# Kernel tuning notes

Measured on AMD Instinct MI355X. Metric: run time of the kernel, lower is better.

The kernel has to match this reference:

```python
import jax, jax.numpy as jnp
import numpy as np

V, H_BASE, D, L, K = 32000, 4096, 512, 2, 4
B = 64

def setup_inputs() -> dict:
    key = jax.random.key(0)
    ks = jax.random.split(key, 12)
    s = 0.02
    return {
        "hidden_state": jax.random.normal(ks[0], (B, H_BASE), jnp.float32),
        "in_proj_w": jax.random.normal(ks[1], (D, H_BASE), jnp.float32) * s,
        "in_proj_b": jnp.zeros((D,), jnp.float32),
        "w_ih0": jax.random.normal(ks[2], (3 * D, D), jnp.float32) * s,
        "w_hh0": jax.random.normal(ks[3], (3 * D, D), jnp.float32) * s,
        "b_ih0": jax.random.normal(ks[4], (3 * D,), jnp.float32) * s,
        "b_hh0": jax.random.normal(ks[5], (3 * D,), jnp.float32) * s,
        "w_ih1": jax.random.normal(ks[6], (3 * D, D), jnp.float32) * s,
        "w_hh1": jax.random.normal(ks[7], (3 * D, D), jnp.float32) * s,
        "b_ih1": jax.random.normal(ks[8], (3 * D,), jnp.float32) * s,
        "b_hh1": jax.random.normal(ks[9], (3 * D,), jnp.float32) * s,
        "embed": jax.random.normal(ks[10], (V, D), jnp.float32) * s,
        "out_w": jax.random.normal(ks[11], (V, D), jnp.float32) * s,
    }

def _gru_cell(x, h, w_ih, w_hh, b_ih, b_hh):
    # PyTorch GRU gate order: r, z, n
    gi = x @ w_ih.T + b_ih  # [B, 3D]
    gh = h @ w_hh.T + b_hh
    ir, iz, inn = jnp.split(gi, 3, axis=-1)
    hr, hz, hn = jnp.split(gh, 3, axis=-1)
    r = jax.nn.sigmoid(ir + hr)
    z = jax.nn.sigmoid(iz + hz)
    n = jnp.tanh(inn + r * hn)
    return (1.0 - z) * n + z * h

def reference(hidden_state, in_proj_w, in_proj_b, w_ih0, w_hh0, b_ih0, b_hh0,
              w_ih1, w_hh1, b_ih1, b_hh1, embed, out_w):
    b = hidden_state.shape[0]
    h0 = hidden_state @ in_proj_w.T + in_proj_b  # [B, D]
    h_l0 = h0
    h_l1 = h0
    x = jnp.zeros((b, in_proj_w.shape[0]), hidden_state.dtype)
    all_logits = []
    for _ in range(K):
        h_l0 = _gru_cell(x, h_l0, w_ih0, w_hh0, b_ih0, b_hh0)
        h_l1 = _gru_cell(h_l0, h_l1, w_ih1, w_hh1, b_ih1, b_hh1)
        logits = h_l1 @ out_w.T  # [B, V]
        all_logits.append(logits)
        x = embed[jnp.argmax(logits, axis=-1)]  # greedy next-token embed
    return jnp.stack(all_logits, axis=1)  # [B, K, V]
```

## Files before the change

### kernel.cpp

```cpp
#include <hip/hip_runtime.h>
#include <math.h>


typedef __attribute__((ext_vector_type(8))) short short8;
typedef __attribute__((ext_vector_type(4))) float f32x4;

__device__ __forceinline__ unsigned short f2bf_rne(float x) {
    unsigned u = __float_as_uint(x);
    unsigned r = (u + 0x7fffu + ((u >> 16) & 1u)) >> 16;
    return (unsigned short)r;
}
__device__ __forceinline__ void split2(float x, unsigned short& hi, unsigned short& lo) {
    unsigned u = __float_as_uint(x);
    hi = (unsigned short)(u >> 16);
    float r = x - __uint_as_float(u & 0xffff0000u);
    lo = f2bf_rne(r);
}

__device__ __forceinline__ void store_plane(unsigned short* hiP, unsigned short* loP,
                                            int m, int d, float v) {
    int s = d >> 6, cl = (d >> 3) & 7, e = d & 7;
    int off = m * 512 + s * 64 + ((cl ^ (m & 7)) * 8) + e;
    unsigned short hi, lo; split2(v, hi, lo);
    hiP[off] = hi; loP[off] = lo;
}

__device__ __forceinline__ void gload16(const void* g, void* lds) {
    __builtin_amdgcn_global_load_lds(
        (const __attribute__((address_space(1))) unsigned int*)g,
        (__attribute__((address_space(3))) unsigned int*)lds, 16, 0, 0);
}

__device__ __forceinline__ void split_w_body(
    const float* __restrict__ W, unsigned short* __restrict__ H,
    unsigned short* __restrict__ L, size_t g, int kclog)
{
    int n  = (int)(g >> kclog);
    int c8 = (int)g & ((1 << kclog) - 1);
    const float* src = W + g * 8;
    float4 v0 = *(const float4*)src;
    float4 v1 = *(const float4*)(src + 4);
    unsigned short h[8], l[8];
    split2(v0.x,h[0],l[0]); split2(v0.y,h[1],l[1]); split2(v0.z,h[2],l[2]); split2(v0.w,h[3],l[3]);
    split2(v1.x,h[4],l[4]); split2(v1.y,h[5],l[5]); split2(v1.z,h[6],l[6]); split2(v1.w,h[7],l[7]);
    uint4 ph = make_uint4((unsigned)h[0]|((unsigned)h[1]<<16), (unsigned)h[2]|((unsigned)h[3]<<16),
                          (unsigned)h[4]|((unsigned)h[5]<<16), (unsigned)h[6]|((unsigned)h[7]<<16));
    uint4 pl = make_uint4((unsigned)l[0]|((unsigned)l[1]<<16), (unsigned)l[2]|((unsigned)l[3]<<16),
                          (unsigned)l[4]|((unsigned)l[5]<<16), (unsigned)l[6]|((unsigned)l[7]<<16));
    int nt = n >> 7, row = n & 127;
    int ksi = c8 >> 3;
    int slot = (c8 & 7) ^ (row & 7);
    int tpr = 1 << (kclog - 3);
    size_t off = ((size_t)(nt * tpr + ksi) * 128 + row) * 64 + slot * 8;
    *(uint4*)(H + off) = ph;
    *(uint4*)(L + off) = pl;
}

__global__ __launch_bounds__(256) void k_split_W(
    const float* __restrict__ W, unsigned short* __restrict__ H,
    unsigned short* __restrict__ L, int kclog)
{
    size_t g = (size_t)blockIdx.x * 256 + threadIdx.x;
    split_w_body(W, H, L, g, kclog);
}

__global__ __launch_bounds__(256) void k_split_gw(
    const float* __restrict__ w0, const float* __restrict__ w1,
    const float* __restrict__ w2, const float* __restrict__ w3,
    unsigned short* __restrict__ H, unsigned short* __restrict__ L)
{
    int mat = blockIdx.y;
    const float* W = mat == 0 ? w0 : mat == 1 ? w1 : mat == 2 ? w2 : w3;
    size_t g = (size_t)blockIdx.x * 256 + threadIdx.x;
    split_w_body(W, H + (size_t)mat * 786432, L + (size_t)mat * 786432, g, 6);
}

template<bool ARGMAX>
__device__ __forceinline__ void mfma_gemm(
    const char* __restrict__ AH, const char* __restrict__ AL, int AstrideB, int akk0,
    const unsigned short* __restrict__ BH, const unsigned short* __restrict__ BL,
    size_t btileU,
    int nk,
    float* __restrict__ C, int ldc, int n0,
    unsigned short (*AsH)[4096], unsigned short (*AsL)[4096],
    unsigned short (*BsH)[8192], unsigned short (*BsL)[8192],
    float* __restrict__ pval, int* __restrict__ pidx, int bx)
{
    const int tid  = threadIdx.x;
    const int wv   = tid >> 6;
    const int lane = tid & 63;
    const int lr   = lane & 15;
    const int lh   = lane >> 4;
    const int m    = tid >> 3;
    const int cp   = tid & 7;

    f32x4 acc[4];
#pragma unroll
    for (int i = 0; i < 4; ++i) acc[i] = (f32x4){0.f, 0.f, 0.f, 0.f};

    auto stage = [&](int t, int p) {
        const int ka = (akk0 + t * 64) * 2;
        gload16(AH + m * AstrideB + ka + cp * 16, (char*)AsH[p] + wv * 1024);
        gload16(AL + m * AstrideB + ka + cp * 16, (char*)AsL[p] + wv * 1024);
        const char* bH = (const char*)BH + (btileU + (size_t)t * 8192) * 2;
        const char* bL = (const char*)BL + (btileU + (size_t)t * 8192) * 2;
        gload16(bH + wv * 2048 +        lane * 16, (char*)BsH[p] + wv * 2048);
        gload16(bH + wv * 2048 + 1024 + lane * 16, (char*)BsH[p] + wv * 2048 + 1024);
        gload16(bL + wv * 2048 +        lane * 16, (char*)BsL[p] + wv * 2048);
        gload16(bL + wv * 2048 + 1024 + lane * 16, (char*)BsL[p] + wv * 2048 + 1024);
    };

    stage(0, 0);
    __syncthreads();

    for (int t = 0; t < nk; ++t) {
        const int p = t & 1;
        if (t + 1 < nk) stage(t + 1, p ^ 1);
#pragma unroll
        for (int kk2 = 0; kk2 < 2; ++kk2) {
            int aoff = lr * 64 + (((kk2 * 4 + lh) ^ (lr & 7)) * 8);
            short8 ah[4], al[4];
#pragma unroll
            for (int mt = 0; mt < 4; ++mt) {
                ah[mt] = *(const short8*)(AsH[p] + mt * 1024 + aoff);
                al[mt] = *(const short8*)(AsL[p] + mt * 1024 + aoff);
            }
            int brow = wv * 16 + lr;
            int boff = brow * 64 + (((kk2 * 4 + lh) ^ (brow & 7)) * 8);
            short8 bh = *(const short8*)(BsH[p] + boff);
            short8 bl = *(const short8*)(BsL[p] + boff);
#pragma unroll
            for (int mt = 0; mt < 4; ++mt) {
                acc[mt] = __builtin_amdgcn_mfma_f32_16x16x32_bf16(ah[mt], bh, acc[mt], 0, 0, 0);
                acc[mt] = __builtin_amdgcn_mfma_f32_16x16x32_bf16(ah[mt], bl, acc[mt], 0, 0, 0);
                acc[mt] = __builtin_amdgcn_mfma_f32_16x16x32_bf16(al[mt], bh, acc[mt], 0, 0, 0);
            }
        }
        __syncthreads();
    }

#pragma unroll
    for (int mt = 0; mt < 4; ++mt)
#pragma unroll
        for (int i = 0; i < 4; ++i) {
            int mm = mt * 16 + lh * 4 + i;
            C[mm * ldc + n0 + wv * 16 + lr] = acc[mt][i];
        }

    if (ARGMAX) {
        float* sv = (float*)&AsH[0][0];
        int*   sc = (int*)&AsL[0][0];
#pragma unroll
        for (int mt = 0; mt < 4; ++mt)
#pragma unroll
            for (int i = 0; i < 4; ++i) {
                float v = acc[mt][i];
                int   c = n0 + wv * 16 + lr;
#pragma unroll
                for (int msk = 1; msk < 16; msk <<= 1) {
                    float ov = __shfl_xor(v, msk, 64);
                    int   oc = __shfl_xor(c, msk, 64);
                    if (ov > v || (ov == v && oc < c)) { v = ov; c = oc; }
                }
                if (lr == 0) {
                    int row = mt * 16 + lh * 4 + i;
                    sv[wv * 64 + row] = v;
                    sc[wv * 64 + row] = c;
                }
            }
        __syncthreads();
        if (tid < 64) {
            float v = sv[tid]; int c = sc[tid];
#pragma unroll
            for (int w = 1; w < 8; ++w) {
                float ov = sv[w * 64 + tid]; int oc = sc[w * 64 + tid];
                if (ov > v) { v = ov; c = oc; }
            }
            pval[bx * 64 + tid] = v;
            pidx[bx * 64 + tid] = c;
        }
    }
}

#define DECLARE_LDS() \
    __shared__ alignas(16) unsigned short AsH[2][4096]; \
    __shared__ alignas(16) unsigned short AsL[2][4096]; \
    __shared__ alignas(16) unsigned short BsH[2][8192]; \
    __shared__ alignas(16) unsigned short BsL[2][8192];

__global__ __launch_bounds__(256) void k_split_A(
    const float* __restrict__ hidden, char* __restrict__ hidH, char* __restrict__ hidL)
{
    int g = blockIdx.x * 256 + threadIdx.x;
    int m = g >> 9;
    int cc = g & 511;
    int s = cc >> 3, cl = cc & 7;
    const float* src = hidden + m * 4096 + cc * 8;
    float4 v0 = *(const float4*)src;
    float4 v1 = *(const float4*)(src + 4);
    unsigned short h[8], l[8];
    split2(v0.x,h[0],l[0]); split2(v0.y,h[1],l[1]); split2(v0.z,h[2],l[2]); split2(v0.w,h[3],l[3]);
    split2(v1.x,h[4],l[4]); split2(v1.y,h[5],l[5]); split2(v1.z,h[6],l[6]); split2(v1.w,h[7],l[7]);
    uint4 ph = make_uint4((unsigned)h[0]|((unsigned)h[1]<<16), (unsigned)h[2]|((unsigned)h[3]<<16),
                          (unsigned)h[4]|((unsigned)h[5]<<16), (unsigned)h[6]|((unsigned)h[7]<<16));
    uint4 pl = make_uint4((unsigned)l[0]|((unsigned)l[1]<<16), (unsigned)l[2]|((unsigned)l[3]<<16),
                          (unsigned)l[4]|((unsigned)l[5]<<16), (unsigned)l[6]|((unsigned)l[7]<<16));
    int off = m * 8192 + s * 128 + ((cl ^ (m & 7)) * 16);
    *(uint4*)(hidH + off) = ph;
    *(uint4*)(hidL + off) = pl;
}

__global__ __launch_bounds__(512) void k_inproj(
    const char* __restrict__ hidH, const char* __restrict__ hidL,
    const unsigned short* __restrict__ WH, const unsigned short* __restrict__ WL,
    float* __restrict__ part)
{
    DECLARE_LDS();
    int nt = blockIdx.x & 3;
    int ks = blockIdx.x >> 2;
    mfma_gemm<false>(hidH, hidL, 8192, ks * 256,
                     WH, WL, (size_t)(nt * 64 + ks * 4) * 8192, 4,
                     part + ks * 32768, 512, nt * 128,
                     AsH, AsL, BsH, BsL, nullptr, nullptr, 0);
}

__global__ __launch_bounds__(256) void k_reduce_inproj(
    const float* __restrict__ part, const float* __restrict__ bias,
    float* __restrict__ hA, float* __restrict__ hB,
    unsigned short* hAH, unsigned short* hAL,
    unsigned short* hBH, unsigned short* hBL,
    unsigned short* xH,  unsigned short* xL)
{
    int i = blockIdx.x * 256 + threadIdx.x;
    int b = i >> 9;
    int d = i & 511;
    float s = bias[d];
#pragma unroll
    for (int ks = 0; ks < 16; ++ks) s += part[ks * 32768 + i];
    hA[i] = s;
    hB[i] = s;
    store_plane(hAH, hAL, b, d, s);
    store_plane(hBH, hBL, b, d, s);
    store_plane(xH,  xL,  b, d, 0.f);
}

__global__ __launch_bounds__(512) void k_gates(
    const char* __restrict__ xH, const char* __restrict__ xL,
    const char* __restrict__ hH, const char* __restrict__ hL,
    const unsigned short* __restrict__ gwH, const unsigned short* __restrict__ gwL,
    int layer, float* __restrict__ gip, float* __restrict__ ghp)
{
    DECLARE_LDS();
    int bx  = blockIdx.x;
    int nt  = bx % 12;
    int ks  = (bx / 12) & 3;
    int mat = bx / 48;
    const char* AH = mat ? hH : xH;
    const char* AL = mat ? hL : xL;
    float* C = (mat ? ghp : gip) + ks * 98304;
    size_t btile = ((size_t)(layer * 2 + mat) * 96 + nt * 8 + ks * 2) * 8192;
    mfma_gemm<false>(AH, AL, 1024, ks * 128,
                     gwH, gwL, btile, 2,
                     C, 1536, nt * 128,
                     AsH, AsL, BsH, BsL, nullptr, nullptr, 0);
}

__global__ __launch_bounds__(256) void k_combine(
    const float* __restrict__ gip, const float* __restrict__ ghp,
    const float* __restrict__ b_ih, const float* __restrict__ b_hh,
    float* __restrict__ h, unsigned short* hH, unsigned short* hL)
{
    int i = blockIdx.x * 256 + threadIdx.x;
    int b = i >> 9;
    int d = i & 511;
    int base = b * 1536 + d;
    float ir = b_ih[d], iz = b_ih[d + 512], inn = b_ih[d + 1024];
    float hr = b_hh[d], hz = b_hh[d + 512], hn = b_hh[d + 1024];
#pragma unroll
    for (int ks = 0; ks < 4; ++ks) {
        const float* gi = gip + ks * 98304 + base;
        const float* gh = ghp + ks * 98304 + base;
        ir  += gi[0];    iz += gi[512];  inn += gi[1024];
        hr  += gh[0];    hz += gh[512];  hn  += gh[1024];
    }
    float r = 1.f / (1.f + expf(-(ir + hr)));
    float z = 1.f / (1.f + expf(-(iz + hz)));
    float n = tanhf(inn + r * hn);
    float hv = (1.f - z) * n + z * h[i];
    h[i] = hv;
    store_plane(hH, hL, b, d, hv);
}

__global__ __launch_bounds__(512) void k_logits(
    const char* __restrict__ hH, const char* __restrict__ hL,
    const unsigned short* __restrict__ WH, const unsigned short* __restrict__ WL,
    float* __restrict__ out, int step,
    float* __restrict__ pval, int* __restrict__ pidx)
{
    DECLARE_LDS();
    mfma_gemm<true>(hH, hL, 1024, 0,
                    WH, WL, (size_t)blockIdx.x * 8 * 8192, 8,
                    out + step * 32000, 128000, blockIdx.x * 128,
                    AsH, AsL, BsH, BsL, pval, pidx, blockIdx.x);
}

__global__ __launch_bounds__(256) void k_reduce_embed(
    const float* __restrict__ pval, const int* __restrict__ pidx,
    const float* __restrict__ embed, unsigned short* xH, unsigned short* xL)
{
    __shared__ float sv[256];
    __shared__ int   sc[256];
    const int b = blockIdx.x;
    const int tid = threadIdx.x;
    float v = -3.4e38f;
    int   c = 0x7fffffff;
    if (tid < 250) { v = pval[tid * 64 + b]; c = pidx[tid * 64 + b]; }
    sv[tid] = v; sc[tid] = c;
    __syncthreads();
    for (int s = 128; s > 0; s >>= 1) {
        if (tid < s) {
            float ov = sv[tid + s]; int oc = sc[tid + s];
            if (ov > sv[tid] || (ov == sv[tid] && oc < sc[tid])) { sv[tid] = ov; sc[tid] = oc; }
        }
        __syncthreads();
    }
    int tok = sc[0];
    for (int j = tid; j < 512; j += 256)
        store_plane(xH, xL, b, j, embed[tok * 512 + j]);
}

extern "C" void kernel_launch(void* const* d_in, const int* in_sizes, int n_in,
                              void* d_out, int out_size, void* d_ws, size_t ws_size,
                              hipStream_t stream)
{
    const float* hidden = (const float*)d_in[0];
    const float* in_w   = (const float*)d_in[1];
    const float* in_b   = (const float*)d_in[2];
    const float* w_ih0  = (const float*)d_in[3];
    const float* w_hh0  = (const float*)d_in[4];
    const float* b_ih0  = (const float*)d_in[5];
    const float* b_hh0  = (const float*)d_in[6];
    const float* w_ih1  = (const float*)d_in[7];
    const float* w_hh1  = (const float*)d_in[8];
    const float* b_ih1  = (const float*)d_in[9];
    const float* b_hh1  = (const float*)d_in[10];
    const float* embed  = (const float*)d_in[11];
    const float* out_w  = (const float*)d_in[12];
    float* out = (float*)d_out;
    char*  ws  = (char*)d_ws;

    float* hA  = (float*)(ws + 0);
    float* hB  = (float*)(ws + 131072);
    unsigned short* xH  = (unsigned short*)(ws + 262144);
    unsigned short* xL  = (unsigned short*)(ws + 327680);
    unsigned short* hAH = (unsigned short*)(ws + 393216);
    unsigned short* hAL = (unsigned short*)(ws + 458752);
    unsigned short* hBH = (unsigned short*)(ws + 524288);
    unsigned short* hBL = (unsigned short*)(ws + 589824);
    char* hidH = ws + 655360;
    char* hidL = ws + 1179648;
    float* gip = (float*)(ws + 1703936);
    float* ghp = (float*)(ws + 3276800);
    float* pval = (float*)(ws + 4849664);
    int*   pidx = (int*)  (ws + 4913664);
    float* ipart = (float*)(ws + 4980736);
    unsigned short* owH = (unsigned short*)(ws + 8388608);
    unsigned short* owL = (unsigned short*)(ws + 41943040);
    unsigned short* gwH = (unsigned short*)(ws + 75497472);
    unsigned short* gwL = (unsigned short*)(ws + 83886080);
    unsigned short* inH = (unsigned short*)(ws + 92274688);
    unsigned short* inL = (unsigned short*)(ws + 96468992);

    k_split_A<<<128, 256, 0, stream>>>(hidden, hidH, hidL);
    k_split_W<<<8000, 256, 0, stream>>>(out_w, owH, owL, 6);
    k_split_gw<<<dim3(384, 4), 256, 0, stream>>>(w_ih0, w_hh0, w_ih1, w_hh1, gwH, gwL);
    k_split_W<<<1024, 256, 0, stream>>>(in_w, inH, inL, 9);
    k_inproj<<<64, 512, 0, stream>>>(hidH, hidL, inH, inL, ipart);
    k_reduce_inproj<<<128, 256, 0, stream>>>(ipart, in_b, hA, hB,
                                             hAH, hAL, hBH, hBL, xH, xL);

    for (int step = 0; step < 4; ++step) {
        k_gates<<<96, 512, 0, stream>>>((char*)xH, (char*)xL, (char*)hAH, (char*)hAL,
                                        gwH, gwL, 0, gip, ghp);
        k_combine<<<128, 256, 0, stream>>>(gip, ghp, b_ih0, b_hh0, hA, hAH, hAL);
        k_gates<<<96, 512, 0, stream>>>((char*)hAH, (char*)hAL, (char*)hBH, (char*)hBL,
                                        gwH, gwL, 1, gip, ghp);
        k_combine<<<128, 256, 0, stream>>>(gip, ghp, b_ih1, b_hh1, hB, hBH, hBL);
        k_logits<<<250, 512, 0, stream>>>((char*)hBH, (char*)hBL, owH, owL,
                                          out, step, pval, pidx);
        k_reduce_embed<<<64, 256, 0, stream>>>(pval, pidx, embed, xH, xL);
    }
}
```

Measured before the change: 361.9 us.

## Fuse split kernels, argmax-embed into gates, and overlap hidden-state gate GEMMs

Merges all weight and activation bf16-splitting launches into one grid-stride kernel. Folds the argmax reduction and embedding gather into the layer-0 input-gate GEMM, and computes the layer-0 and layer-1 recurrent-gate GEMMs in the same launch. It also splits K more finely so more blocks run (256 in-proj blocks, 8-way gate partials), and skips the x@W_ih GEMM at step 0 since x is zero. This cuts launches and serial dependencies per step, at the cost of more partial-sum traffic in the combine and reduce kernels.

```diff
diff --git a/kernel.cpp b/kernel.cpp
--- a/kernel.cpp
+++ b/kernel.cpp
@@ -56,142 +56,10 @@
     *(uint4*)(L + off) = pl;
 }
 
-__global__ __launch_bounds__(256) void k_split_W(
-    const float* __restrict__ W, unsigned short* __restrict__ H,
-    unsigned short* __restrict__ L, int kclog)
-{
-    size_t g = (size_t)blockIdx.x * 256 + threadIdx.x;
-    split_w_body(W, H, L, g, kclog);
-}
-
-__global__ __launch_bounds__(256) void k_split_gw(
-    const float* __restrict__ w0, const float* __restrict__ w1,
-    const float* __restrict__ w2, const float* __restrict__ w3,
-    unsigned short* __restrict__ H, unsigned short* __restrict__ L)
-{
-    int mat = blockIdx.y;
-    const float* W = mat == 0 ? w0 : mat == 1 ? w1 : mat == 2 ? w2 : w3;
-    size_t g = (size_t)blockIdx.x * 256 + threadIdx.x;
-    split_w_body(W, H + (size_t)mat * 786432, L + (size_t)mat * 786432, g, 6);
-}
-
-template<bool ARGMAX>
-__device__ __forceinline__ void mfma_gemm(
-    const char* __restrict__ AH, const char* __restrict__ AL, int AstrideB, int akk0,
-    const unsigned short* __restrict__ BH, const unsigned short* __restrict__ BL,
-    size_t btileU,
-    int nk,
-    float* __restrict__ C, int ldc, int n0,
-    unsigned short (*AsH)[4096], unsigned short (*AsL)[4096],
-    unsigned short (*BsH)[8192], unsigned short (*BsL)[8192],
-    float* __restrict__ pval, int* __restrict__ pidx, int bx)
-{
-    const int tid  = threadIdx.x;
-    const int wv   = tid >> 6;
-    const int lane = tid & 63;
-    const int lr   = lane & 15;
-    const int lh   = lane >> 4;
-    const int m    = tid >> 3;
-    const int cp   = tid & 7;
-
-    f32x4 acc[4];
-#pragma unroll
-    for (int i = 0; i < 4; ++i) acc[i] = (f32x4){0.f, 0.f, 0.f, 0.f};
-
-    auto stage = [&](int t, int p) {
-        const int ka = (akk0 + t * 64) * 2;
-        gload16(AH + m * AstrideB + ka + cp * 16, (char*)AsH[p] + wv * 1024);
-        gload16(AL + m * AstrideB + ka + cp * 16, (char*)AsL[p] + wv * 1024);
-        const char* bH = (const char*)BH + (btileU + (size_t)t * 8192) * 2;
-        const char* bL = (const char*)BL + (btileU + (size_t)t * 8192) * 2;
-        gload16(bH + wv * 2048 +        lane * 16, (char*)BsH[p] + wv * 2048);
-        gload16(bH + wv * 2048 + 1024 + lane * 16, (char*)BsH[p] + wv * 2048 + 1024);
-        gload16(bL + wv * 2048 +        lane * 16, (char*)BsL[p] + wv * 2048);
-        gload16(bL + wv * 2048 + 1024 + lane * 16, (char*)BsL[p] + wv * 2048 + 1024);
-    };
-
-    stage(0, 0);
-    __syncthreads();
-
-    for (int t = 0; t < nk; ++t) {
-        const int p = t & 1;
-        if (t + 1 < nk) stage(t + 1, p ^ 1);
-#pragma unroll
-        for (int kk2 = 0; kk2 < 2; ++kk2) {
-            int aoff = lr * 64 + (((kk2 * 4 + lh) ^ (lr & 7)) * 8);
-            short8 ah[4], al[4];
-#pragma unroll
-            for (int mt = 0; mt < 4; ++mt) {
-                ah[mt] = *(const short8*)(AsH[p] + mt * 1024 + aoff);
-                al[mt] = *(const short8*)(AsL[p] + mt * 1024 + aoff);
-            }
-            int brow = wv * 16 + lr;
-            int boff = brow * 64 + (((kk2 * 4 + lh) ^ (brow & 7)) * 8);
-            short8 bh = *(const short8*)(BsH[p] + boff);
-            short8 bl = *(const short8*)(BsL[p] + boff);
-#pragma unroll
-            for (int mt = 0; mt < 4; ++mt) {
-                acc[mt] = __builtin_amdgcn_mfma_f32_16x16x32_bf16(ah[mt], bh, acc[mt], 0, 0, 0);
-                acc[mt] = __builtin_amdgcn_mfma_f32_16x16x32_bf16(ah[mt], bl, acc[mt], 0, 0, 0);
-                acc[mt] = __builtin_amdgcn_mfma_f32_16x16x32_bf16(al[mt], bh, acc[mt], 0, 0, 0);
-            }
-        }
-        __syncthreads();
-    }
-
-#pragma unroll
-    for (int mt = 0; mt < 4; ++mt)
-#pragma unroll
-        for (int i = 0; i < 4; ++i) {
-            int mm = mt * 16 + lh * 4 + i;
-            C[mm * ldc + n0 + wv * 16 + lr] = acc[mt][i];
-        }
-
-    if (ARGMAX) {
-        float* sv = (float*)&AsH[0][0];
-        int*   sc = (int*)&AsL[0][0];
-#pragma unroll
-        for (int mt = 0; mt < 4; ++mt)
-#pragma unroll
-            for (int i = 0; i < 4; ++i) {
-                float v = acc[mt][i];
-                int   c = n0 + wv * 16 + lr;
-#pragma unroll
-                for (int msk = 1; msk < 16; msk <<= 1) {
-                    float ov = __shfl_xor(v, msk, 64);
-                    int   oc = __shfl_xor(c, msk, 64);
-                    if (ov > v || (ov == v && oc < c)) { v = ov; c = oc; }
-                }
-                if (lr == 0) {
-                    int row = mt * 16 + lh * 4 + i;
-                    sv[wv * 64 + row] = v;
-                    sc[wv * 64 + row] = c;
-                }
-            }
-        __syncthreads();
-        if (tid < 64) {
-            float v = sv[tid]; int c = sc[tid];
-#pragma unroll
-            for (int w = 1; w < 8; ++w) {
-                float ov = sv[w * 64 + tid]; int oc = sc[w * 64 + tid];
-                if (ov > v) { v = ov; c = oc; }
-            }
-            pval[bx * 64 + tid] = v;
-            pidx[bx * 64 + tid] = c;
-        }
-    }
-}
-
-#define DECLARE_LDS() \
-    __shared__ alignas(16) unsigned short AsH[2][4096]; \
-    __shared__ alignas(16) unsigned short AsL[2][4096]; \
-    __shared__ alignas(16) unsigned short BsH[2][8192]; \
-    __shared__ alignas(16) unsigned short BsL[2][8192];
-
-__global__ __launch_bounds__(256) void k_split_A(
-    const float* __restrict__ hidden, char* __restrict__ hidH, char* __restrict__ hidL)
-{
-    int g = blockIdx.x * 256 + threadIdx.x;
+__device__ __forceinline__ void split_a_body(
+    const float* __restrict__ hidden, char* __restrict__ hidH,
+    char* __restrict__ hidL, int g)
+{
     int m = g >> 9;
     int cc = g & 511;
     int s = cc >> 3, cl = cc & 7;
@@ -210,78 +78,317 @@
     *(uint4*)(hidL + off) = pl;
 }
 
+__device__ __forceinline__ void mfma_core(
+    const unsigned short* __restrict__ AsH0, const unsigned short* __restrict__ AsL0,
+    const unsigned short* __restrict__ BsH0, const unsigned short* __restrict__ BsL0,
+    int wv, int lr, int lh, f32x4* acc)
+{
+#pragma unroll
+    for (int kk2 = 0; kk2 < 2; ++kk2) {
+        int aoff = lr * 64 + (((kk2 * 4 + lh) ^ (lr & 7)) * 8);
+        short8 ah[4], al[4];
+#pragma unroll
+        for (int mt = 0; mt < 4; ++mt) {
+            ah[mt] = *(const short8*)(AsH0 + mt * 1024 + aoff);
+            al[mt] = *(const short8*)(AsL0 + mt * 1024 + aoff);
+        }
+        int brow = wv * 16 + lr;
+        int boff = brow * 64 + (((kk2 * 4 + lh) ^ (brow & 7)) * 8);
+        short8 bh = *(const short8*)(BsH0 + boff);
+        short8 bl = *(const short8*)(BsL0 + boff);
+#pragma unroll
+        for (int mt = 0; mt < 4; ++mt) {
+            acc[mt] = __builtin_amdgcn_mfma_f32_16x16x32_bf16(ah[mt], bh, acc[mt], 0, 0, 0);
+            acc[mt] = __builtin_amdgcn_mfma_f32_16x16x32_bf16(ah[mt], bl, acc[mt], 0, 0, 0);
+            acc[mt] = __builtin_amdgcn_mfma_f32_16x16x32_bf16(al[mt], bh, acc[mt], 0, 0, 0);
+        }
+    }
+}
+
+__device__ __forceinline__ void epilogue_write(
+    float* __restrict__ C, int ldc, int n0, int wv, int lr, int lh, const f32x4* acc)
+{
+#pragma unroll
+    for (int mt = 0; mt < 4; ++mt)
+#pragma unroll
+        for (int i = 0; i < 4; ++i) {
+            int mm = mt * 16 + lh * 4 + i;
+            C[mm * ldc + n0 + wv * 16 + lr] = acc[mt][i];
+        }
+}
+
+template<bool ARGMAX>
+__device__ __forceinline__ void mfma_gemm(
+    const char* __restrict__ AH, const char* __restrict__ AL, int AstrideB, int akk0,
+    const unsigned short* __restrict__ BH, const unsigned short* __restrict__ BL,
+    size_t btileU, int nk,
+    float* __restrict__ C, int ldc, int n0,
+    unsigned short (*AsH)[4096], unsigned short (*AsL)[4096],
+    unsigned short (*BsH)[8192], unsigned short (*BsL)[8192],
+    float* __restrict__ pval, int* __restrict__ pidx, int bx)
+{
+    const int tid  = threadIdx.x;
+    const int wv   = tid >> 6;
+    const int lane = tid & 63;
+    const int lr   = lane & 15;
+    const int lh   = lane >> 4;
+    const int m    = tid >> 3;
+    const int cp   = tid & 7;
+
+    f32x4 acc[4];
+#pragma unroll
+    for (int i = 0; i < 4; ++i) acc[i] = (f32x4){0.f, 0.f, 0.f, 0.f};
+
+    auto stage = [&](int t, int p) {
+        const int ka = (akk0 + t * 64) * 2;
+        gload16(AH + m * AstrideB + ka + cp * 16, (char*)AsH[p] + wv * 1024);
+        gload16(AL + m * AstrideB + ka + cp * 16, (char*)AsL[p] + wv * 1024);
+        const char* bH = (const char*)BH + (btileU + (size_t)t * 8192) * 2;
+        const char* bL = (const char*)BL + (btileU + (size_t)t * 8192) * 2;
+        gload16(bH + wv * 2048 +        lane * 16, (char*)BsH[p] + wv * 2048);
+        gload16(bH + wv * 2048 + 1024 + lane * 16, (char*)BsH[p] + wv * 2048 + 1024);
+        gload16(bL + wv * 2048 +        lane * 16, (char*)BsL[p] + wv * 2048);
+        gload16(bL + wv * 2048 + 1024 + lane * 16, (char*)BsL[p] + wv * 2048 + 1024);
+    };
+
+    stage(0, 0);
+    __syncthreads();
+
+    for (int t = 0; t < nk; ++t) {
+        const int p = t & 1;
+        if (t + 1 < nk) stage(t + 1, p ^ 1);
+        mfma_core(AsH[p], AsL[p], BsH[p], BsL[p], wv, lr, lh, acc);
+        __syncthreads();
+    }
+
+    epilogue_write(C, ldc, n0, wv, lr, lh, acc);
+
+    if (ARGMAX) {
+        float* sv = (float*)&AsH[0][0];
+        int*   sc = (int*)&AsL[0][0];
+#pragma unroll
+        for (int mt = 0; mt < 4; ++mt)
+#pragma unroll
+            for (int i = 0; i < 4; ++i) {
+                float v = acc[mt][i];
+                int   c = n0 + wv * 16 + lr;
+#pragma unroll
+                for (int msk = 1; msk < 16; msk <<= 1) {
+                    float ov = __shfl_xor(v, msk, 64);
+                    int   oc = __shfl_xor(c, msk, 64);
+                    if (ov > v || (ov == v && oc < c)) { v = ov; c = oc; }
+                }
+                if (lr == 0) {
+                    int row = mt * 16 + lh * 4 + i;
+                    sv[wv * 64 + row] = v;
+                    sc[wv * 64 + row] = c;
+                }
+            }
+        __syncthreads();
+        if (tid < 64) {
+            float v = sv[tid]; int c = sc[tid];
+#pragma unroll
+            for (int w = 1; w < 8; ++w) {
+                float ov = sv[w * 64 + tid]; int oc = sc[w * 64 + tid];
+                if (ov > v) { v = ov; c = oc; }
+            }
+            pval[bx * 64 + tid] = v;
+            pidx[bx * 64 + tid] = c;
+        }
+    }
+}
+
+#define DECLARE_LDS() \
+    __shared__ alignas(16) unsigned short AsH[2][4096]; \
+    __shared__ alignas(16) unsigned short AsL[2][4096]; \
+    __shared__ alignas(16) unsigned short BsH[2][8192]; \
+    __shared__ alignas(16) unsigned short BsL[2][8192];
+
+__global__ __launch_bounds__(512) void k_split_all(
+    const float* __restrict__ out_w, const float* __restrict__ w_ih0,
+    const float* __restrict__ w_hh0, const float* __restrict__ w_ih1,
+    const float* __restrict__ w_hh1, const float* __restrict__ in_w,
+    const float* __restrict__ hidden,
+    unsigned short* __restrict__ owH, unsigned short* __restrict__ owL,
+    unsigned short* __restrict__ gwH, unsigned short* __restrict__ gwL,
+    unsigned short* __restrict__ inH, unsigned short* __restrict__ inL,
+    char* __restrict__ hidH, char* __restrict__ hidL)
+{
+    size_t gt = (size_t)blockIdx.x * 512 + threadIdx.x;
+    for (size_t u = gt; u < 2736128; u += 131072) {
+        if (u < 2048000) {
+            split_w_body(out_w, owH, owL, u, 6);
+        } else if (u < 2441216) {
+            size_t g = u - 2048000;
+            int mat = (int)(g / 98304);
+            const float* W = mat == 0 ? w_ih0 : mat == 1 ? w_hh0
+                           : mat == 2 ? w_ih1 : w_hh1;
+            split_w_body(W, gwH + (size_t)mat * 786432, gwL + (size_t)mat * 786432,
+                         g % 98304, 6);
+        } else if (u < 2703360) {
+            split_w_body(in_w, inH, inL, u - 2441216, 9);
+        } else {
+            split_a_body(hidden, hidH, hidL, (int)(u - 2703360));
+        }
+    }
+}
+
 __global__ __launch_bounds__(512) void k_inproj(
     const char* __restrict__ hidH, const char* __restrict__ hidL,
-    const unsigned short* __restrict__ WH, const unsigned short* __restrict__ WL,
-    float* __restrict__ part)
+    const unsigned short* __restrict__ inH, const unsigned short* __restrict__ inL,
+    float* __restrict__ ipart)
 {
     DECLARE_LDS();
     int nt = blockIdx.x & 3;
     int ks = blockIdx.x >> 2;
-    mfma_gemm<false>(hidH, hidL, 8192, ks * 256,
-                     WH, WL, (size_t)(nt * 64 + ks * 4) * 8192, 4,
-                     part + ks * 32768, 512, nt * 128,
+    mfma_gemm<false>(hidH, hidL, 8192, ks * 64,
+                     inH, inL, (size_t)(nt * 64 + ks) * 8192, 1,
+                     ipart + ks * 32768, 512, nt * 128,
                      AsH, AsL, BsH, BsL, nullptr, nullptr, 0);
 }
 
-__global__ __launch_bounds__(256) void k_reduce_inproj(
-    const float* __restrict__ part, const float* __restrict__ bias,
+__global__ __launch_bounds__(512) void k_reduce_inproj(
+    const float* __restrict__ ipart, const float* __restrict__ bias,
     float* __restrict__ hA, float* __restrict__ hB,
     unsigned short* hAH, unsigned short* hAL,
-    unsigned short* hBH, unsigned short* hBL,
-    unsigned short* xH,  unsigned short* xL)
-{
-    int i = blockIdx.x * 256 + threadIdx.x;
+    unsigned short* hBH, unsigned short* hBL)
+{
+    int i = blockIdx.x * 512 + threadIdx.x;
     int b = i >> 9;
     int d = i & 511;
     float s = bias[d];
-#pragma unroll
-    for (int ks = 0; ks < 16; ++ks) s += part[ks * 32768 + i];
+#pragma unroll 8
+    for (int ks = 0; ks < 64; ++ks) s += ipart[ks * 32768 + i];
     hA[i] = s;
     hB[i] = s;
     store_plane(hAH, hAL, b, d, s);
     store_plane(hBH, hBL, b, d, s);
-    store_plane(xH,  xL,  b, d, 0.f);
-}
-
-__global__ __launch_bounds__(512) void k_gates(
-    const char* __restrict__ xH, const char* __restrict__ xL,
-    const char* __restrict__ hH, const char* __restrict__ hL,
+}
+
+__global__ __launch_bounds__(512) void k_gates3(
+    int step,
+    const float* __restrict__ pval, const int* __restrict__ pidx,
+    const float* __restrict__ embed,
+    const char* __restrict__ hAH, const char* __restrict__ hAL,
+    const char* __restrict__ hBH, const char* __restrict__ hBL,
     const unsigned short* __restrict__ gwH, const unsigned short* __restrict__ gwL,
-    int layer, float* __restrict__ gip, float* __restrict__ ghp)
+    float* __restrict__ gi0, float* __restrict__ gh0, float* __restrict__ gh1)
 {
     DECLARE_LDS();
-    int bx  = blockIdx.x;
-    int nt  = bx % 12;
-    int ks  = (bx / 12) & 3;
-    int mat = bx / 48;
-    const char* AH = mat ? hH : xH;
-    const char* AL = mat ? hL : xL;
-    float* C = (mat ? ghp : gip) + ks * 98304;
-    size_t btile = ((size_t)(layer * 2 + mat) * 96 + nt * 8 + ks * 2) * 8192;
-    mfma_gemm<false>(AH, AL, 1024, ks * 128,
-                     gwH, gwL, btile, 2,
-                     C, 1536, nt * 128,
+    const int bx  = blockIdx.x;
+    const int tid = threadIdx.x;
+
+    if (bx < 96) {
+        int nt = bx % 12, ks = bx / 12;
+        float* C = gi0 + ks * 98304;
+        if (step == 0) {
+            float4 z = make_float4(0.f, 0.f, 0.f, 0.f);
+            for (int q = tid; q < 2048; q += 512) {
+                int r = q >> 4, cq = q & 15;
+                *(float4*)(C + r * 1536 + nt * 128 + cq * 4) = z;
+            }
+            return;
+        }
+        const int wv = tid >> 6, lane = tid & 63, lr = lane & 15, lh = lane >> 4;
+        size_t btileU = ((size_t)nt * 8 + ks) * 8192;
+        const char* bH = (const char*)gwH + btileU * 2;
+        const char* bL = (const char*)gwL + btileU * 2;
+        gload16(bH + wv * 2048 +        lane * 16, (char*)BsH[0] + wv * 2048);
+        gload16(bH + wv * 2048 + 1024 + lane * 16, (char*)BsH[0] + wv * 2048 + 1024);
+        gload16(bL + wv * 2048 +        lane * 16, (char*)BsL[0] + wv * 2048);
+        gload16(bL + wv * 2048 + 1024 + lane * 16, (char*)BsL[0] + wv * 2048 + 1024);
+        int r = tid >> 3, j0 = tid & 7;
+        float v = -3.4e38f; int c = 0x7fffffff;
+        for (int j = j0; j < 250; j += 8) {
+            float ov = pval[j * 64 + r]; int oc = pidx[j * 64 + r];
+            if (ov > v || (ov == v && oc < c)) { v = ov; c = oc; }
+        }
+#pragma unroll
+        for (int msk = 1; msk < 8; msk <<= 1) {
+            float ov = __shfl_xor(v, msk, 64);
+            int   oc = __shfl_xor(c, msk, 64);
+            if (ov > v || (ov == v && oc < c)) { v = ov; c = oc; }
+        }
+        int* stok = (int*)AsH[1];
+        if (j0 == 0) stok[r] = c;
+        __syncthreads();
+        {
+            int mm = tid >> 3, cp = tid & 7;
+            int tok = stok[mm];
+            const float* src = embed + (size_t)tok * 512 + ks * 64 + cp * 8;
+            float4 v0 = *(const float4*)src;
+            float4 v1 = *(const float4*)(src + 4);
+            unsigned short h[8], l[8];
+            split2(v0.x,h[0],l[0]); split2(v0.y,h[1],l[1]); split2(v0.z,h[2],l[2]); split2(v0.w,h[3],l[3]);
+            split2(v1.x,h[4],l[4]); split2(v1.y,h[5],l[5]); split2(v1.z,h[6],l[6]); split2(v1.w,h[7],l[7]);
+            uint4 ph = make_uint4((unsigned)h[0]|((unsigned)h[1]<<16), (unsigned)h[2]|((unsigned)h[3]<<16),
+                                  (unsigned)h[4]|((unsigned)h[5]<<16), (unsigned)h[6]|((unsigned)h[7]<<16));
+            uint4 pl = make_uint4((unsigned)l[0]|((unsigned)l[1]<<16), (unsigned)l[2]|((unsigned)l[3]<<16),
+                                  (unsigned)l[4]|((unsigned)l[5]<<16), (unsigned)l[6]|((unsigned)l[7]<<16));
+            int off = mm * 64 + ((cp ^ (mm & 7)) * 8);
+            *(uint4*)(AsH[0] + off) = ph;
+            *(uint4*)(AsL[0] + off) = pl;
+        }
+        __syncthreads();
+        f32x4 acc[4];
+#pragma unroll
+        for (int i = 0; i < 4; ++i) acc[i] = (f32x4){0.f, 0.f, 0.f, 0.f};
+        mfma_core(AsH[0], AsL[0], BsH[0], BsL[0], wv, lr, lh, acc);
+        epilogue_write(C, 1536, nt * 128, wv, lr, lh, acc);
+    } else if (bx < 192) {
+        int idx = bx - 96;
+        int nt = idx % 12, ks = idx / 12;
+        size_t btile = ((size_t)96 + nt * 8 + ks) * 8192;
+        mfma_gemm<false>((const char*)hAH, (const char*)hAL, 1024, ks * 64,
+                         gwH, gwL, btile, 1,
+                         gh0 + ks * 98304, 1536, nt * 128,
+                         AsH, AsL, BsH, BsL, nullptr, nullptr, 0);
+    } else {
+        int idx = bx - 192;
+        int nt = idx % 12, ks2 = idx / 12;
+        size_t btile = ((size_t)288 + nt * 8 + ks2 * 2) * 8192;
+        mfma_gemm<false>((const char*)hBH, (const char*)hBL, 1024, ks2 * 128,
+                         gwH, gwL, btile, 2,
+                         gh1 + ks2 * 98304, 1536, nt * 128,
+                         AsH, AsL, BsH, BsL, nullptr, nullptr, 0);
+    }
+}
+
+__global__ __launch_bounds__(512) void k_gates1(
+    const char* __restrict__ hAH, const char* __restrict__ hAL,
+    const unsigned short* __restrict__ gwH, const unsigned short* __restrict__ gwL,
+    float* __restrict__ gi1)
+{
+    DECLARE_LDS();
+    int nt = blockIdx.x % 12, ks = blockIdx.x / 12;
+    size_t btile = ((size_t)192 + nt * 8 + ks) * 8192;
+    mfma_gemm<false>((const char*)hAH, (const char*)hAL, 1024, ks * 64,
+                     gwH, gwL, btile, 1,
+                     gi1 + ks * 98304, 1536, nt * 128,
                      AsH, AsL, BsH, BsL, nullptr, nullptr, 0);
 }
 
-__global__ __launch_bounds__(256) void k_combine(
-    const float* __restrict__ gip, const float* __restrict__ ghp,
+template<int NGI, int NGH>
+__global__ __launch_bounds__(512) void k_combine(
+    const float* __restrict__ gi, const float* __restrict__ gh,
     const float* __restrict__ b_ih, const float* __restrict__ b_hh,
     float* __restrict__ h, unsigned short* hH, unsigned short* hL)
 {
-    int i = blockIdx.x * 256 + threadIdx.x;
+    int i = blockIdx.x * 512 + threadIdx.x;
     int b = i >> 9;
     int d = i & 511;
     int base = b * 1536 + d;
     float ir = b_ih[d], iz = b_ih[d + 512], inn = b_ih[d + 1024];
     float hr = b_hh[d], hz = b_hh[d + 512], hn = b_hh[d + 1024];
 #pragma unroll
-    for (int ks = 0; ks < 4; ++ks) {
-        const float* gi = gip + ks * 98304 + base;
-        const float* gh = ghp + ks * 98304 + base;
-        ir  += gi[0];    iz += gi[512];  inn += gi[1024];
-        hr  += gh[0];    hz += gh[512];  hn  += gh[1024];
+    for (int ks = 0; ks < NGI; ++ks) {
+        const float* g = gi + ks * 98304 + base;
+        ir += g[0]; iz += g[512]; inn += g[1024];
+    }
+#pragma unroll
+    for (int ks = 0; ks < NGH; ++ks) {
+        const float* g = gh + ks * 98304 + base;
+        hr += g[0]; hz += g[512]; hn += g[1024];
     }
     float r = 1.f / (1.f + expf(-(ir + hr)));
     float z = 1.f / (1.f + expf(-(iz + hz)));
@@ -302,31 +409,6 @@
                     WH, WL, (size_t)blockIdx.x * 8 * 8192, 8,
                     out + step * 32000, 128000, blockIdx.x * 128,
                     AsH, AsL, BsH, BsL, pval, pidx, blockIdx.x);
-}
-
-__global__ __launch_bounds__(256) void k_reduce_embed(
-    const float* __restrict__ pval, const int* __restrict__ pidx,
-    const float* __restrict__ embed, unsigned short* xH, unsigned short* xL)
-{
-    __shared__ float sv[256];
-    __shared__ int   sc[256];
-    const int b = blockIdx.x;
-    const int tid = threadIdx.x;
-    float v = -3.4e38f;
-    int   c = 0x7fffffff;
-    if (tid < 250) { v = pval[tid * 64 + b]; c = pidx[tid * 64 + b]; }
-    sv[tid] = v; sc[tid] = c;
-    __syncthreads();
-    for (int s = 128; s > 0; s >>= 1) {
-        if (tid < s) {
-            float ov = sv[tid + s]; int oc = sc[tid + s];
-            if (ov > sv[tid] || (ov == sv[tid] && oc < sc[tid])) { sv[tid] = ov; sc[tid] = oc; }
-        }
-        __syncthreads();
-    }
-    int tok = sc[0];
-    for (int j = tid; j < 512; j += 256)
-        store_plane(xH, xL, b, j, embed[tok * 512 + j]);
 }
 
 extern "C" void kernel_launch(void* const* d_in, const int* in_sizes, int n_in,
@@ -351,43 +433,44 @@
 
     float* hA  = (float*)(ws + 0);
     float* hB  = (float*)(ws + 131072);
-    unsigned short* xH  = (unsigned short*)(ws + 262144);
-    unsigned short* xL  = (unsigned short*)(ws + 327680);
-    unsigned short* hAH = (unsigned short*)(ws + 393216);
-    unsigned short* hAL = (unsigned short*)(ws + 458752);
-    unsigned short* hBH = (unsigned short*)(ws + 524288);
-    unsigned short* hBL = (unsigned short*)(ws + 589824);
-    char* hidH = ws + 655360;
-    char* hidL = ws + 1179648;
-    float* gip = (float*)(ws + 1703936);
-    float* ghp = (float*)(ws + 3276800);
-    float* pval = (float*)(ws + 4849664);
-    int*   pidx = (int*)  (ws + 4913664);
-    float* ipart = (float*)(ws + 4980736);
-    unsigned short* owH = (unsigned short*)(ws + 8388608);
-    unsigned short* owL = (unsigned short*)(ws + 41943040);
-    unsigned short* gwH = (unsigned short*)(ws + 75497472);
-    unsigned short* gwL = (unsigned short*)(ws + 83886080);
-    unsigned short* inH = (unsigned short*)(ws + 92274688);
-    unsigned short* inL = (unsigned short*)(ws + 96468992);
-
-    k_split_A<<<128, 256, 0, stream>>>(hidden, hidH, hidL);
-    k_split_W<<<8000, 256, 0, stream>>>(out_w, owH, owL, 6);
-    k_split_gw<<<dim3(384, 4), 256, 0, stream>>>(w_ih0, w_hh0, w_ih1, w_hh1, gwH, gwL);
-    k_split_W<<<1024, 256, 0, stream>>>(in_w, inH, inL, 9);
-    k_inproj<<<64, 512, 0, stream>>>(hidH, hidL, inH, inL, ipart);
-    k_reduce_inproj<<<128, 256, 0, stream>>>(ipart, in_b, hA, hB,
-                                             hAH, hAL, hBH, hBL, xH, xL);
+    unsigned short* hAH = (unsigned short*)(ws + 262144);
+    unsigned short* hAL = (unsigned short*)(ws + 327680);
+    unsigned short* hBH = (unsigned short*)(ws + 393216);
+    unsigned short* hBL = (unsigned short*)(ws + 458752);
+    char* hidH = ws + 524288;
+    char* hidL = ws + 1048576;
+    float* g_gi0 = (float*)(ws + 1572864);
+    float* g_gh0 = (float*)(ws + 4718592);
+    float* g_gi1 = (float*)(ws + 7864320);
+    float* g_gh1 = (float*)(ws + 11010048);
+    float* pval  = (float*)(ws + 12582912);
+    int*   pidx  = (int*)  (ws + 12648448);
+    float* ipart = (float*)(ws + 12713984);
+    unsigned short* owH = (unsigned short*)(ws + 21102592);
+    unsigned short* owL = (unsigned short*)(ws + 53870592);
+    unsigned short* gwH = (unsigned short*)(ws + 86638592);
+    unsigned short* gwL = (unsigned short*)(ws + 92930048);
+    unsigned short* inH = (unsigned short*)(ws + 99221504);
+    unsigned short* inL = (unsigned short*)(ws + 103415808);
+
+    k_split_all<<<256, 512, 0, stream>>>(out_w, w_ih0, w_hh0, w_ih1, w_hh1,
+                                         in_w, hidden,
+                                         owH, owL, gwH, gwL, inH, inL, hidH, hidL);
+    k_inproj<<<256, 512, 0, stream>>>(hidH, hidL, inH, inL, ipart);
+    k_reduce_inproj<<<64, 512, 0, stream>>>(ipart, in_b, hA, hB,
+                                            hAH, hAL, hBH, hBL);
 
     for (int step = 0; step < 4; ++step) {
-        k_gates<<<96, 512, 0, stream>>>((char*)xH, (char*)xL, (char*)hAH, (char*)hAL,
-                                        gwH, gwL, 0, gip, ghp);
-        k_combine<<<128, 256, 0, stream>>>(gip, ghp, b_ih0, b_hh0, hA, hAH, hAL);
-        k_gates<<<96, 512, 0, stream>>>((char*)hAH, (char*)hAL, (char*)hBH, (char*)hBL,
-                                        gwH, gwL, 1, gip, ghp);
-        k_combine<<<128, 256, 0, stream>>>(gip, ghp, b_ih1, b_hh1, hB, hBH, hBL);
+        k_gates3<<<240, 512, 0, stream>>>(step, pval, pidx, embed,
+                                          (char*)hAH, (char*)hAL,
+                                          (char*)hBH, (char*)hBL,
+                                          gwH, gwL, g_gi0, g_gh0, g_gh1);
+        k_combine<8, 8><<<64, 512, 0, stream>>>(g_gi0, g_gh0, b_ih0, b_hh0,
+                                                hA, hAH, hAL);
+        k_gates1<<<96, 512, 0, stream>>>((char*)hAH, (char*)hAL, gwH, gwL, g_gi1);
+        k_combine<8, 4><<<64, 512, 0, stream>>>(g_gi1, g_gh1, b_ih1, b_hh1,
+                                                hB, hBH, hBL);
         k_logits<<<250, 512, 0, stream>>>((char*)hBH, (char*)hBL, owH, owL,
                                           out, step, pval, pidx);
-        k_reduce_embed<<<64, 256, 0, stream>>>(pval, pidx, embed, xH, xL);
-    }
-}
+    }
+}
```

Measured after the change: 370.4 us. 2.3% more time.
